# Kernel tuning notes

Hardware: AMD Instinct MI355X
Metric: run time of the kernel (lower is better)

## Reference

```python
import jax, jax.numpy as jnp
import numpy as np

B, S, V = 256, 8, 32000
PLACEHOLDER = -1


def setup_inputs() -> dict:
    key = jax.random.key(0)
    ks = jax.random.split(key, 8)
    rng = np.random.default_rng(0)
    lens = rng.integers(1, S + 1, size=B)          # ragged draft lengths per request
    cu = np.cumsum(lens).astype(np.int32)
    N = int(cu[-1])
    draft_token_ids = jax.random.randint(ks[0], (N,), 0, V, dtype=jnp.int32)
    dp = jax.random.uniform(ks[1], (N, V), dtype=jnp.float32)
    draft_probs = dp / dp.sum(-1, keepdims=True)
    tp = jax.random.uniform(ks[2], (N, V), dtype=jnp.float32)
    target_probs = tp / tp.sum(-1, keepdims=True)
    bonus_token_ids = jax.random.randint(ks[3], (B,), 0, V, dtype=jnp.int32)
    uniform_probs = jax.random.uniform(ks[4], (N,), dtype=jnp.float32)
    is_greedy = jax.random.uniform(ks[5], (B,)) < 0.5
    q = jax.random.exponential(ks[6], (B, V), dtype=jnp.float32)  # Gumbel-trick noise
    return dict(draft_probs=draft_probs, target_probs=target_probs,
                uniform_probs=uniform_probs, q=q,
                cu_num_draft_tokens=jnp.asarray(cu), draft_token_ids=draft_token_ids,
                bonus_token_ids=bonus_token_ids, is_greedy=is_greedy, max_spec_len=S)


def reference(draft_probs, target_probs, uniform_probs, q,
              cu_num_draft_tokens, draft_token_ids, bonus_token_ids,
              is_greedy, max_spec_len):
    cu = cu_num_draft_tokens
    b = cu.shape[0]
    n = draft_token_ids.shape[0]
    s = int(max_spec_len)
    starts = jnp.concatenate([jnp.zeros((1,), cu.dtype), cu[:-1]])
    lens = cu - starts                                   # [B]
    tok_idx = jnp.arange(n)
    tok_req = jnp.searchsorted(cu, tok_idx, side='right')  # [N] request id per token
    pos = tok_idx - starts[tok_req]                        # [N] position within request

    # greedy branch: accept while draft matches target argmax, emit target argmax
    target_argmax = jnp.argmax(target_probs, axis=-1).astype(jnp.int32)  # [N]

    # random branch: accept iff draft_prob>0 and target/draft >= u
    d_at = draft_probs[tok_idx, draft_token_ids]
    t_at = target_probs[tok_idx, draft_token_ids]
    rnd_accept = (d_at > 0) & (t_at >= uniform_probs * d_at)

    # recovered tokens: argmax over vocab of max(target-draft,0)/q (exp-noise sampling)
    recovered = jnp.argmax(jnp.maximum(target_probs - draft_probs, 0.0) / q[tok_req],
                           axis=-1).astype(jnp.int32)     # [N]

    greedy_t = is_greedy[tok_req]
    accept = jnp.where(greedy_t, draft_token_ids == target_argmax, rnd_accept)
    token = jnp.where(greedy_t, target_argmax,
                      jnp.where(rnd_accept, draft_token_ids, recovered))

    # densify ragged tokens to [B, S]; padding positions count as accepted
    dense_acc = jnp.ones((b, s), bool).at[tok_req, pos].set(accept)
    dense_val = jnp.zeros((b, s), bool).at[tok_req, pos].set(True)
    dense_tok = jnp.full((b, s), PLACEHOLDER, jnp.int32).at[tok_req, pos].set(token)

    # early-exit scan: position p is written iff all positions < p were accepted
    cm = jnp.cumprod(dense_acc.astype(jnp.int32), axis=1).astype(bool)
    excl = jnp.concatenate([jnp.ones((b, 1), bool), cm[:, :-1]], axis=1)
    write = excl & dense_val
    body = jnp.where(write, dense_tok, PLACEHOLDER)
    out = jnp.concatenate([body, jnp.full((b, 1), PLACEHOLDER, jnp.int32)], axis=1)

    # bonus token if every draft token was accepted
    rows = jnp.arange(b)
    out = out.at[rows, lens].set(jnp.where(cm[:, -1], bonus_token_ids, out[rows, lens]))
    return out
```

## Files before the change

### kernel.cpp

```cpp
#include <hip/hip_runtime.h>

#define PLACEHOLDER (-1)
#define T 1024
#define NW (T / 64)

__device__ __forceinline__ void comb(float& v, int& i, float v2, int i2) {
    if (v2 > v || (v2 == v && i2 < i)) { v = v2; i = i2; }
}

__device__ int block_argmax(float bv, int bi, float* s_v, int* s_i) {
    #pragma unroll
    for (int off = 32; off > 0; off >>= 1) {
        float v2 = __shfl_down(bv, off);
        int   i2 = __shfl_down(bi, off);
        comb(bv, bi, v2, i2);
    }
    const int tid = threadIdx.x;
    if ((tid & 63) == 0) { s_v[tid >> 6] = bv; s_i[tid >> 6] = bi; }
    __syncthreads();
    if (tid == 0) {
        for (int w = 1; w < NW; ++w) comb(bv, bi, s_v[w], s_i[w]);
        s_i[0] = bi;
    }
    __syncthreads();
    int r = s_i[0];
    __syncthreads();
    return r;
}

__global__ __launch_bounds__(T) void fused_kernel(
    const float* __restrict__ dp, const float* __restrict__ tp,
    const float* __restrict__ up, const float* __restrict__ q,
    const int* __restrict__ cu, const int* __restrict__ did,
    const int* __restrict__ bonus, const void* __restrict__ grd,
    int* __restrict__ out, int B, int V, int S)
{
    const int b   = blockIdx.x;
    const int tid = threadIdx.x;

    __shared__ float s_v[NW];
    __shared__ int   s_i[NW];
    __shared__ int   s_flags[2];
    __shared__ int   sh_tok, sh_acc;

    if (tid < 2) s_flags[tid] = 0;
    __syncthreads();
    const unsigned char* gb = (const unsigned char*)grd;
    if (tid < B) {
        unsigned char c = gb[tid];
        if (c > 1) s_flags[0] = 1;
        if ((tid & 3) && c) s_flags[1] = 1;
    }
    __syncthreads();
    bool g;
    if (s_flags[0])      g = (((const float*)grd)[b] != 0.0f);
    else if (s_flags[1]) g = (gb[b] != 0);
    else                 g = (((const int*)grd)[b] != 0);

    const int start = (b == 0) ? 0 : cu[b - 1];
    const int len   = cu[b] - start;
    int* row = out + b * (S + 1);

    const int V4 = V >> 2;
    bool allacc = true;
    int  p = 0;
    for (; p < len; ++p) {
        const int i = start + p;
        const float* __restrict__ trow = tp + (size_t)i * V;
        int tok, acc;
        if (g) {
            float bv = -1.0f; int bi = 0;
            const float4* t4 = (const float4*)trow;
            for (int j = tid; j < V4; j += T) {
                float4 t = t4[j]; const int base = j << 2;
                if (t.x > bv) { bv = t.x; bi = base;     }
                if (t.y > bv) { bv = t.y; bi = base + 1; }
                if (t.z > bv) { bv = t.z; bi = base + 2; }
                if (t.w > bv) { bv = t.w; bi = base + 3; }
            }
            for (int j = (V4 << 2) + tid; j < V; j += T) {
                float tv = trow[j];
                if (tv > bv) { bv = tv; bi = j; }
            }
            tok = block_argmax(bv, bi, s_v, s_i);
            acc = (did[i] == tok) ? 1 : 0;
        } else {
            __syncthreads();
            if (tid == 0) {
                const int td    = did[i];
                const float dat = dp[(size_t)i * V + td];
                const float tat = trow[td];
                sh_acc = (dat > 0.0f && tat >= up[i] * dat) ? 1 : 0;
                sh_tok = td;
            }
            __syncthreads();
            acc = sh_acc;
            tok = sh_tok;
            if (!acc) {
                const float4* t4 = (const float4*)trow;
                const float4* d4 = (const float4*)(dp + (size_t)i * V);
                const float4* q4 = (const float4*)(q  + (size_t)b * V);
                float bv = -1.0f; int bi = 0;
                for (int j = tid; j < V4; j += T) {
                    float4 t = t4[j], d = d4[j], qq = q4[j];
                    const int base = j << 2;
                    float r;
                    r = fmaxf(t.x - d.x, 0.0f) / qq.x; if (r > bv) { bv = r; bi = base;     }
                    r = fmaxf(t.y - d.y, 0.0f) / qq.y; if (r > bv) { bv = r; bi = base + 1; }
                    r = fmaxf(t.z - d.z, 0.0f) / qq.z; if (r > bv) { bv = r; bi = base + 2; }
                    r = fmaxf(t.w - d.w, 0.0f) / qq.w; if (r > bv) { bv = r; bi = base + 3; }
                }
                for (int j = (V4 << 2) + tid; j < V; j += T) {
                    float r = fmaxf(trow[j] - dp[(size_t)i * V + j], 0.0f)
                              / q[(size_t)b * V + j];
                    if (r > bv) { bv = r; bi = j; }
                }
                tok = block_argmax(bv, bi, s_v, s_i);
            }
        }
        if (tid == 0) row[p] = tok;
        if (!acc) { allacc = false; ++p; break; }
    }
    if (tid == 0) {
        for (int r = p; r <= S; ++r) row[r] = PLACEHOLDER;
        if (allacc) row[len] = bonus[b];
    }
}

extern "C" void kernel_launch(void* const* d_in, const int* in_sizes, int n_in,
                              void* d_out, int out_size, void* d_ws, size_t ws_size,
                              hipStream_t stream) {
    const float* dp  = (const float*)d_in[0];
    const float* tp  = (const float*)d_in[1];
    const float* up  = (const float*)d_in[2];
    const float* q   = (const float*)d_in[3];
    const int*   cu  = (const int*)d_in[4];
    const int*   did = (const int*)d_in[5];
    const int*   bon = (const int*)d_in[6];
    const void*  grd = d_in[7];

    const int B = in_sizes[4];
    const int N = in_sizes[5];
    const int V = in_sizes[0] / N;
    const int S = out_size / B - 1;

    fused_kernel<<<B, T, 0, stream>>>(dp, tp, up, q, cu, did, bon, grd,
                                      (int*)d_out, B, V, S);
}
```

Before: 20.80 us.

## Split fused kernel into prepass, multi-block sliced argmax scan, and finish

Replaces the single per-request kernel with three launches. A prepass computes all random-branch acceptances at once with a wavefront ballot and writes accepted tokens directly. A sliced scan kernel spreads each request's first vocabulary argmax over several blocks and combines them with a packed 64-bit atomicMax. A finish kernel writes the recovered token or continues the serial greedy argmax for later positions. The goal is more parallelism and removing the serial per-token loop for sampled requests, at the cost of extra launch overhead, workspace traffic and atomics.

```diff
diff --git a/kernel.cpp b/kernel.cpp
--- a/kernel.cpp
+++ b/kernel.cpp
@@ -1,14 +1,13 @@
 #include <hip/hip_runtime.h>
 
 #define PLACEHOLDER (-1)
-#define T 1024
-#define NW (T / 64)
+#define KB 8
 
 __device__ __forceinline__ void comb(float& v, int& i, float v2, int i2) {
     if (v2 > v || (v2 == v && i2 < i)) { v = v2; i = i2; }
 }
 
-__device__ int block_argmax(float bv, int bi, float* s_v, int* s_i) {
+__device__ __forceinline__ void block_argmax(float& bv, int& bi, float* s_v, int* s_i) {
     #pragma unroll
     for (int off = 32; off > 0; off >>= 1) {
         float v2 = __shfl_down(bv, off);
@@ -16,114 +15,194 @@
         comb(bv, bi, v2, i2);
     }
     const int tid = threadIdx.x;
+    const int nw  = blockDim.x >> 6;
     if ((tid & 63) == 0) { s_v[tid >> 6] = bv; s_i[tid >> 6] = bi; }
     __syncthreads();
     if (tid == 0) {
-        for (int w = 1; w < NW; ++w) comb(bv, bi, s_v[w], s_i[w]);
-        s_i[0] = bi;
-    }
-    __syncthreads();
-    int r = s_i[0];
-    __syncthreads();
-    return r;
-}
-
-__global__ __launch_bounds__(T) void fused_kernel(
-    const float* __restrict__ dp, const float* __restrict__ tp,
-    const float* __restrict__ up, const float* __restrict__ q,
-    const int* __restrict__ cu, const int* __restrict__ did,
-    const int* __restrict__ bonus, const void* __restrict__ grd,
-    int* __restrict__ out, int B, int V, int S)
-{
-    const int b   = blockIdx.x;
+        for (int w = 1; w < nw; ++w) comb(bv, bi, s_v[w], s_i[w]);
+        s_v[0] = bv; s_i[0] = bi;
+    }
+    __syncthreads();
+    bv = s_v[0]; bi = s_i[0];
+    __syncthreads();
+}
+
+__device__ __forceinline__ bool detect_greedy(const void* grd, int b, int B, int* s_flags) {
     const int tid = threadIdx.x;
-
-    __shared__ float s_v[NW];
-    __shared__ int   s_i[NW];
-    __shared__ int   s_flags[2];
-    __shared__ int   sh_tok, sh_acc;
-
     if (tid < 2) s_flags[tid] = 0;
     __syncthreads();
     const unsigned char* gb = (const unsigned char*)grd;
-    if (tid < B) {
-        unsigned char c = gb[tid];
+    for (int t = tid; t < B; t += blockDim.x) {
+        unsigned char c = gb[t];
         if (c > 1) s_flags[0] = 1;
-        if ((tid & 3) && c) s_flags[1] = 1;
+        if ((t & 3) && c) s_flags[1] = 1;
     }
     __syncthreads();
     bool g;
     if (s_flags[0])      g = (((const float*)grd)[b] != 0.0f);
     else if (s_flags[1]) g = (gb[b] != 0);
     else                 g = (((const int*)grd)[b] != 0);
-
-    const int start = (b == 0) ? 0 : cu[b - 1];
+    return g;
+}
+
+__device__ __forceinline__ unsigned long long pack_vi(float v, int i) {
+    return ((unsigned long long)__float_as_uint(v) << 32)
+         | (unsigned long long)(0xFFFFFFFFu - (unsigned)i);
+}
+
+__global__ __launch_bounds__(64) void k1_prepass(
+    const float* __restrict__ dp, const float* __restrict__ tp,
+    const float* __restrict__ up, const int* __restrict__ cu,
+    const int* __restrict__ did, const int* __restrict__ bonus,
+    const void* __restrict__ grd, int* __restrict__ out,
+    int* __restrict__ scanrow, int* __restrict__ scankind,
+    unsigned long long* __restrict__ packed, int B, int V, int S)
+{
+    __shared__ int s_flags[2];
+    const int b = blockIdx.x, tid = threadIdx.x;
+    const bool g = detect_greedy(grd, b, B, s_flags);
+    const int start = b ? cu[b - 1] : 0;
+    const int len   = cu[b] - start;
+
+    bool acc = true;
+    if (tid < len) {
+        const int i  = start + tid;
+        const int td = did[i];
+        const float dat = dp[(size_t)i * V + td];
+        const float tat = tp[(size_t)i * V + td];
+        acc = (dat > 0.0f && tat >= up[i] * dat);
+    }
+    const unsigned long long rej =
+        (~__ballot(acc)) & ((len >= 64) ? ~0ull : ((1ull << len) - 1ull));
+
+    if (tid == 0) {
+        packed[b] = 0xFFFFFFFFull;
+        int* row = out + b * (S + 1);
+        if (g) {
+            scanrow[b] = start; scankind[b] = 1;
+        } else {
+            const int fr = rej ? (__ffsll((long long)rej) - 1) : len;
+            for (int p = 0; p < fr; ++p) row[p] = did[start + p];
+            if (fr < len) {
+                scanrow[b] = start + fr; scankind[b] = 0;
+                for (int p = fr + 1; p <= S; ++p) row[p] = PLACEHOLDER;
+            } else {
+                scanrow[b] = -1; scankind[b] = 0;
+                row[len] = bonus[b];
+                for (int p = len + 1; p <= S; ++p) row[p] = PLACEHOLDER;
+            }
+        }
+    }
+}
+
+__global__ __launch_bounds__(256) void k3_scan(
+    const float* __restrict__ dp, const float* __restrict__ tp,
+    const float* __restrict__ q, const int* __restrict__ scanrow,
+    const int* __restrict__ scankind, unsigned long long* __restrict__ packed,
+    int V)
+{
+    const int bq = blockIdx.x / KB, slice = blockIdx.x % KB;
+    const int row = scanrow[bq];
+    if (row < 0) return;
+    const int tid = threadIdx.x;
+    __shared__ float s_v[4];
+    __shared__ int   s_i[4];
+
+    const int V4 = V >> 2;
+    const int c4 = (V4 + KB - 1) / KB;
+    const int j0 = slice * c4;
+    const int j1 = min(j0 + c4, V4);
+
+    float bv = 0.0f; int bi = 0x7FFFFFFF;
+    if (scankind[bq]) {
+        const float4* t4 = (const float4*)(tp + (size_t)row * V);
+        for (int j = j0 + tid; j < j1; j += 256) {
+            const float4 t = t4[j]; const int base = j << 2;
+            if (t.x > bv) { bv = t.x; bi = base;     }
+            if (t.y > bv) { bv = t.y; bi = base + 1; }
+            if (t.z > bv) { bv = t.z; bi = base + 2; }
+            if (t.w > bv) { bv = t.w; bi = base + 3; }
+        }
+        if (slice == KB - 1)
+            for (int j = (V4 << 2) + tid; j < V; j += 256) {
+                const float tv = tp[(size_t)row * V + j];
+                if (tv > bv) { bv = tv; bi = j; }
+            }
+    } else {
+        const float4* t4 = (const float4*)(tp + (size_t)row * V);
+        const float4* d4 = (const float4*)(dp + (size_t)row * V);
+        const float4* q4 = (const float4*)(q  + (size_t)bq  * V);
+        for (int j = j0 + tid; j < j1; j += 256) {
+            const float4 t = t4[j], d = d4[j], qq = q4[j];
+            const int base = j << 2;
+            float r;
+            r = fmaxf(t.x - d.x, 0.0f) / qq.x; if (r > bv) { bv = r; bi = base;     }
+            r = fmaxf(t.y - d.y, 0.0f) / qq.y; if (r > bv) { bv = r; bi = base + 1; }
+            r = fmaxf(t.z - d.z, 0.0f) / qq.z; if (r > bv) { bv = r; bi = base + 2; }
+            r = fmaxf(t.w - d.w, 0.0f) / qq.w; if (r > bv) { bv = r; bi = base + 3; }
+        }
+        if (slice == KB - 1)
+            for (int j = (V4 << 2) + tid; j < V; j += 256) {
+                const float r = fmaxf(tp[(size_t)row * V + j] - dp[(size_t)row * V + j], 0.0f)
+                                / q[(size_t)bq * V + j];
+                if (r > bv) { bv = r; bi = j; }
+            }
+    }
+    block_argmax(bv, bi, s_v, s_i);
+    if (tid == 0) atomicMax(&packed[bq], pack_vi(bv, bi));
+}
+
+__global__ __launch_bounds__(1024) void k4_finish(
+    const float* __restrict__ tp, const int* __restrict__ cu,
+    const int* __restrict__ did, const int* __restrict__ bonus,
+    const void* __restrict__ grd, const int* __restrict__ scanrow,
+    const unsigned long long* __restrict__ packed,
+    int* __restrict__ out, int B, int V, int S)
+{
+    __shared__ int   s_flags[2];
+    __shared__ float s_v[16];
+    __shared__ int   s_i[16];
+    const int b = blockIdx.x, tid = threadIdx.x;
+    const bool g = detect_greedy(grd, b, B, s_flags);
+    const int start = b ? cu[b - 1] : 0;
     const int len   = cu[b] - start;
     int* row = out + b * (S + 1);
 
+    if (!g) {
+        const int sr = scanrow[b];
+        if (sr >= 0 && tid == 0) {
+            const unsigned long long pk = packed[b];
+            row[sr - start] = (int)(0xFFFFFFFFu - (unsigned)(pk & 0xFFFFFFFFull));
+        }
+        return;
+    }
+    const unsigned long long pk = packed[b];
+    const int tok0 = (int)(0xFFFFFFFFu - (unsigned)(pk & 0xFFFFFFFFull));
+    if (tid == 0) row[0] = tok0;
+    bool ok = (did[start] == tok0);
+    int p = 1;
     const int V4 = V >> 2;
-    bool allacc = true;
-    int  p = 0;
-    for (; p < len; ++p) {
-        const int i = start + p;
-        const float* __restrict__ trow = tp + (size_t)i * V;
-        int tok, acc;
-        if (g) {
-            float bv = -1.0f; int bi = 0;
-            const float4* t4 = (const float4*)trow;
-            for (int j = tid; j < V4; j += T) {
-                float4 t = t4[j]; const int base = j << 2;
-                if (t.x > bv) { bv = t.x; bi = base;     }
-                if (t.y > bv) { bv = t.y; bi = base + 1; }
-                if (t.z > bv) { bv = t.z; bi = base + 2; }
-                if (t.w > bv) { bv = t.w; bi = base + 3; }
-            }
-            for (int j = (V4 << 2) + tid; j < V; j += T) {
-                float tv = trow[j];
-                if (tv > bv) { bv = tv; bi = j; }
-            }
-            tok = block_argmax(bv, bi, s_v, s_i);
-            acc = (did[i] == tok) ? 1 : 0;
-        } else {
-            __syncthreads();
-            if (tid == 0) {
-                const int td    = did[i];
-                const float dat = dp[(size_t)i * V + td];
-                const float tat = trow[td];
-                sh_acc = (dat > 0.0f && tat >= up[i] * dat) ? 1 : 0;
-                sh_tok = td;
-            }
-            __syncthreads();
-            acc = sh_acc;
-            tok = sh_tok;
-            if (!acc) {
-                const float4* t4 = (const float4*)trow;
-                const float4* d4 = (const float4*)(dp + (size_t)i * V);
-                const float4* q4 = (const float4*)(q  + (size_t)b * V);
-                float bv = -1.0f; int bi = 0;
-                for (int j = tid; j < V4; j += T) {
-                    float4 t = t4[j], d = d4[j], qq = q4[j];
-                    const int base = j << 2;
-                    float r;
-                    r = fmaxf(t.x - d.x, 0.0f) / qq.x; if (r > bv) { bv = r; bi = base;     }
-                    r = fmaxf(t.y - d.y, 0.0f) / qq.y; if (r > bv) { bv = r; bi = base + 1; }
-                    r = fmaxf(t.z - d.z, 0.0f) / qq.z; if (r > bv) { bv = r; bi = base + 2; }
-                    r = fmaxf(t.w - d.w, 0.0f) / qq.w; if (r > bv) { bv = r; bi = base + 3; }
-                }
-                for (int j = (V4 << 2) + tid; j < V; j += T) {
-                    float r = fmaxf(trow[j] - dp[(size_t)i * V + j], 0.0f)
-                              / q[(size_t)b * V + j];
-                    if (r > bv) { bv = r; bi = j; }
-                }
-                tok = block_argmax(bv, bi, s_v, s_i);
-            }
-        }
-        if (tid == 0) row[p] = tok;
-        if (!acc) { allacc = false; ++p; break; }
+    for (; p < len && ok; ++p) {
+        const float4* t4 = (const float4*)(tp + (size_t)(start + p) * V);
+        float bv = 0.0f; int bi = 0x7FFFFFFF;
+        for (int j = tid; j < V4; j += 1024) {
+            const float4 t = t4[j]; const int base = j << 2;
+            if (t.x > bv) { bv = t.x; bi = base;     }
+            if (t.y > bv) { bv = t.y; bi = base + 1; }
+            if (t.z > bv) { bv = t.z; bi = base + 2; }
+            if (t.w > bv) { bv = t.w; bi = base + 3; }
+        }
+        for (int j = (V4 << 2) + tid; j < V; j += 1024) {
+            const float tv = tp[(size_t)(start + p) * V + j];
+            if (tv > bv) { bv = tv; bi = j; }
+        }
+        block_argmax(bv, bi, s_v, s_i);
+        if (tid == 0) row[p] = bi;
+        ok = (did[start + p] == bi);
     }
     if (tid == 0) {
         for (int r = p; r <= S; ++r) row[r] = PLACEHOLDER;
-        if (allacc) row[len] = bonus[b];
+        if (ok) row[len] = bonus[b];
     }
 }
 
@@ -144,6 +223,13 @@
     const int V = in_sizes[0] / N;
     const int S = out_size / B - 1;
 
-    fused_kernel<<<B, T, 0, stream>>>(dp, tp, up, q, cu, did, bon, grd,
+    int* scanrow  = (int*)d_ws;
+    int* scankind = scanrow + B;
+    unsigned long long* packed = (unsigned long long*)(scanrow + 2 * B);
+
+    k1_prepass<<<B, 64, 0, stream>>>(dp, tp, up, cu, did, bon, grd,
+                                     (int*)d_out, scanrow, scankind, packed, B, V, S);
+    k3_scan<<<B * KB, 256, 0, stream>>>(dp, tp, q, scanrow, scankind, packed, V);
+    k4_finish<<<B, 1024, 0, stream>>>(tp, cu, did, bon, grd, scanrow, packed,
                                       (int*)d_out, B, V, S);
 }
```

Result: slower. 23.93 us (+15.0%).
